# Kernel optimization log

Measured on AMD Instinct MI355X. Metric: run time of the kernel, lower is better.

## Reference

```python
import jax, jax.numpy as jnp
import numpy as np

NUM_GRAPHS = 512


def setup_inputs() -> dict:
    key = jax.random.key(0)
    k1, k2, k3, k4, k5, k6, k7 = jax.random.split(key, 7)
    N, E, D_IN, D_H = 100000, 3200000, 384, 64
    x_sem = jax.random.normal(k1, (N, D_IN), dtype=jnp.float32)
    edge_index = jax.random.randint(k2, (2, E), 0, N, dtype=jnp.int64)
    batch_index = jnp.sort(jax.random.randint(k3, (N,), 0, NUM_GRAPHS, dtype=jnp.int64))
    # GCNConv params: linear (no bias) + separate bias; classifier Linear(D_H, 1)
    W_gcn = jax.random.normal(k4, (D_IN, D_H), dtype=jnp.float32) / np.sqrt(D_IN)
    b_gcn = jnp.zeros((D_H,), dtype=jnp.float32)
    W_cls = jax.random.normal(k5, (D_H, 1), dtype=jnp.float32) / np.sqrt(D_H)
    b_cls = jnp.zeros((1,), dtype=jnp.float32)
    return {"x_sem": x_sem, "edge_index": edge_index, "batch_index": batch_index,
            "W_gcn": W_gcn, "b_gcn": b_gcn, "W_cls": W_cls, "b_cls": b_cls}


def reference(x_sem, edge_index, batch_index, W_gcn, b_gcn, W_cls, b_cls):
    N = x_sem.shape[0]
    # GCNConv: add self-loops, symmetric deg^{-1/2} A deg^{-1/2} normalization
    loop = jnp.arange(N, dtype=edge_index.dtype)
    src = jnp.concatenate([edge_index[0], loop])  # message source (x_j)
    dst = jnp.concatenate([edge_index[1], loop])  # aggregation target
    deg = jax.ops.segment_sum(jnp.ones_like(dst, dtype=x_sem.dtype), dst, num_segments=N)
    deg_inv_sqrt = jnp.where(deg > 0, jax.lax.rsqrt(jnp.maximum(deg, 1.0)), 0.0)
    norm = deg_inv_sqrt[src] * deg_inv_sqrt[dst]  # [E+N]
    h = x_sem @ W_gcn                                       # [N, D_H] project first (cheaper)
    msg = h[src] * norm[:, None]                            # gather + scale
    agg = jax.ops.segment_sum(msg, dst, num_segments=N) + b_gcn
    h = jax.nn.relu(agg)
    # global_add_pool over sorted batch_index
    z_graph = jax.ops.segment_sum(h, batch_index, num_segments=NUM_GRAPHS)  # [G, D_H]
    logits = z_graph @ W_cls + b_cls                        # [G, 1]
    return jnp.squeeze(logits, axis=-1)                     # [G]
```

## Files before the change

### kernel.cpp

```cpp
#include <hip/hip_runtime.h>
#include <hip/hip_bf16.h>

#define D_IN 384
#define D_H  64
#define BSH  7
#define BN   128
#define NBLK 512
#define EBUF 4608

typedef __attribute__((ext_vector_type(8))) short short8;
typedef __attribute__((ext_vector_type(4))) float f32x4;

__device__ __forceinline__ unsigned f2bf(float f){
  unsigned u = __float_as_uint(f);
  u += 0x7fffu + ((u >> 16) & 1u);
  return u >> 16;
}
__device__ __forceinline__ float bf2f(unsigned short u){
  return __uint_as_float((unsigned)u << 16);
}

__global__ __launch_bounds__(256) void k_bcount2(const int* __restrict__ ei,
                                                 int* __restrict__ hists,
                                                 int E, int NB, int chunk){
  __shared__ int hist[1024];
  const int blk = blockIdx.x;
  const int t = threadIdx.x;
  for (int i = t; i < NB; i += 256) hist[i] = 0;
  __syncthreads();
  const int cs = blk * chunk;
  const int ce = min(E, cs + chunk);
  for (int e = cs + t; e < ce; e += 256)
    atomicAdd(&hist[ei[E + e] >> BSH], 1);
  __syncthreads();
  for (int i = t; i < NB; i += 256)
    hists[(size_t)blk * NB + i] = hist[i];
}

__global__ __launch_bounds__(NBLK) void k_blkscan(const int* __restrict__ hists,
                                                  int* __restrict__ offs,
                                                  int* __restrict__ bsum, int NB){
  __shared__ int sd[NBLK];
  const int b = blockIdx.x;
  const int t = threadIdx.x;
  int c = hists[(size_t)t * NB + b];
  sd[t] = c;
  __syncthreads();
  for (int off = 1; off < NBLK; off <<= 1){
    int v = (t >= off) ? sd[t - off] : 0;
    __syncthreads();
    sd[t] += v;
    __syncthreads();
  }
  offs[(size_t)b * NBLK + t] = sd[t] - c;
  if (t == NBLK - 1) bsum[b] = sd[t];
}

__global__ __launch_bounds__(1024) void k_bscan(const int* __restrict__ bsum,
                                                int* bstart, int NB, int E){
  __shared__ int sd[1024];
  int t = threadIdx.x;
  int c = (t < NB) ? bsum[t] : 0;
  sd[t] = c;
  __syncthreads();
  for (int off = 1; off < 1024; off <<= 1){
    int v = (t >= off) ? sd[t - off] : 0;
    __syncthreads();
    sd[t] += v;
    __syncthreads();
  }
  if (t < NB) bstart[t] = sd[t] - c;
  if (t == 0) bstart[NB] = E;
}

__global__ __launch_bounds__(256) void k_bscatter2(const int* __restrict__ ei,
                                                   const int* __restrict__ bstart,
                                                   const int* __restrict__ offs,
                                                   unsigned* __restrict__ bscat,
                                                   int E, int NB, int chunk){
  __shared__ int lcur[1024];
  const int blk = blockIdx.x;
  const int t = threadIdx.x;
  for (int i = t; i < NB; i += 256)
    lcur[i] = bstart[i] + offs[(size_t)i * NBLK + blk];
  __syncthreads();
  const int cs = blk * chunk;
  const int ce = min(E, cs + chunk);
  for (int e = cs + t; e < ce; e += 256){
    int s = ei[e];
    int d = ei[E + e];
    int b = d >> BSH;
    int pos = atomicAdd(&lcur[b], 1);
    bscat[pos] = ((unsigned)(d & (BN - 1)) << 17) | (unsigned)s;
  }
}

__global__ __launch_bounds__(256) void k_nodecsr(const unsigned* __restrict__ bscat,
                                                 const int* __restrict__ bstart,
                                                 int* __restrict__ csr,
                                                 int* __restrict__ rowstart,
                                                 float* __restrict__ dis,
                                                 int N, int NB, int E){
  __shared__ int lcnt[BN];
  __shared__ int sc[BN];
  __shared__ int lcur[BN];
  __shared__ unsigned ebuf[EBUF];
  const int b = blockIdx.x;
  const int t = threadIdx.x;
  const int es = bstart[b], ee = bstart[b + 1];
  const int cnt = ee - es;

  if (t < BN) lcnt[t] = 0;
  __syncthreads();
  for (int i = t; i < cnt; i += 256){
    unsigned p = bscat[es + i];
    if (i < EBUF) ebuf[i] = p;
    atomicAdd(&lcnt[p >> 17], 1);
  }
  __syncthreads();
  if (t < BN) sc[t] = lcnt[t];
  __syncthreads();
  for (int off = 1; off < BN; off <<= 1){
    int v = (t < BN && t >= off) ? sc[t - off] : 0;
    __syncthreads();
    if (t < BN) sc[t] += v;
    __syncthreads();
  }
  if (t < BN){
    int excl = sc[t] - lcnt[t];
    lcur[t] = excl;
    int node = b * BN + t;
    if (node < N){
      rowstart[node] = es + excl;
      dis[node] = rsqrtf((float)(lcnt[t] + 1));
    }
  }
  if (b == NB - 1 && t == 0) rowstart[N] = E;
  __syncthreads();
  for (int i = t; i < cnt; i += 256){
    unsigned p = (i < EBUF) ? ebuf[i] : bscat[es + i];
    int pos = atomicAdd(&lcur[p >> 17], 1);
    csr[es + pos] = (int)((p & 0x1FFFFu) << 7);
  }
}

__global__ void k_wconv(const float* __restrict__ W, uint4* __restrict__ bpre){
  int j = blockIdx.x * blockDim.x + threadIdx.x;
  if (j >= 3072) return;
  int id = j & 1023, c = j >> 10;
  int cl = id & 63, s = (id >> 6) & 3, tl = id >> 8;
  int k = c * 128 + s * 32 + ((cl >> 4) << 3);
  int n = tl * 16 + (cl & 15);
  const float* wp = &W[(size_t)k * D_H + n];
  uint4 qv;
  qv.x = f2bf(wp[0])   | (f2bf(wp[64])  << 16);
  qv.y = f2bf(wp[128]) | (f2bf(wp[192]) << 16);
  qv.z = f2bf(wp[256]) | (f2bf(wp[320]) << 16);
  qv.w = f2bf(wp[384]) | (f2bf(wp[448]) << 16);
  bpre[j] = qv;
}

__global__ __launch_bounds__(256) void k_gemm(const float* __restrict__ x,
                                              const uint4* __restrict__ bpre,
                                              const float* __restrict__ dis,
                                              unsigned short* __restrict__ hb, int N){
  const int t = threadIdx.x;
  const int w = t >> 6;
  const int l = t & 63;
  const int node0 = blockIdx.x * 64;
  const int row = node0 + w * 16 + (l & 15);
  const int rowc = row < N ? row : N - 1;
  const float* xr = x + (size_t)rowc * D_IN + ((l >> 4) << 3);

  f32x4 acc[4];
  #pragma unroll
  for (int nt = 0; nt < 4; nt++) acc[nt] = (f32x4){0.f, 0.f, 0.f, 0.f};

  #pragma unroll
  for (int c = 0; c < 3; c++){
    #pragma unroll
    for (int s = 0; s < 4; s++){
      const float* xp = xr + c * 128 + s * 32;
      float4 u0 = *(const float4*)xp;
      float4 u1 = *(const float4*)(xp + 4);
      uint4 pv;
      pv.x = f2bf(u0.x) | (f2bf(u0.y) << 16);
      pv.y = f2bf(u0.z) | (f2bf(u0.w) << 16);
      pv.z = f2bf(u1.x) | (f2bf(u1.y) << 16);
      pv.w = f2bf(u1.z) | (f2bf(u1.w) << 16);
      short8 a = *reinterpret_cast<short8*>(&pv);
      #pragma unroll
      for (int nt = 0; nt < 4; nt++){
        short8 b = *reinterpret_cast<const short8*>(&bpre[c * 1024 + (nt * 4 + s) * 64 + l]);
        acc[nt] = __builtin_amdgcn_mfma_f32_16x16x32_bf16(a, b, acc[nt], 0, 0, 0);
      }
    }
  }
  const int qd = l >> 4;
  const int col0 = l & 15;
  #pragma unroll
  for (int r = 0; r < 4; r++){
    int node = node0 + w * 16 + qd * 4 + r;
    if (node < N){
      float scale = dis[node];
      #pragma unroll
      for (int nt = 0; nt < 4; nt++)
        hb[(size_t)node * D_H + nt * 16 + col0] = (unsigned short)f2bf(acc[nt][r] * scale);
    }
  }
}

__global__ __launch_bounds__(256) void k_agg(const unsigned short* __restrict__ hb,
                                             const int* __restrict__ csr,
                                             const int* __restrict__ rowstart,
                                             const float* __restrict__ dis,
                                             const float* __restrict__ bg,
                                             float* __restrict__ hout, int N){
  int gid = blockIdx.x * 256 + (int)threadIdx.x;
  int i = __builtin_amdgcn_readfirstlane(gid >> 6);
  if (i >= N) return;
  const int l = threadIdx.x & 63;
  const int c4 = (l & 31) << 2;
  const int hsel = l >> 5;
  const char* hbb = (const char*)hb;
  float ax = 0.f, ay = 0.f;

  {
    unsigned u = *(const unsigned*)(hbb + ((size_t)(unsigned)i << 7) + c4);
    if (!hsel){
      ax += __uint_as_float(u << 16);
      ay += __uint_as_float(u & 0xffff0000u);
    }
  }
  int e = rowstart[i];
  const int re = rowstart[i + 1];
  for (; e + 8 <= re; e += 8){
    int b0 = csr[e + 0], b1 = csr[e + 1];
    int b2 = csr[e + 2], b3 = csr[e + 3];
    int b4 = csr[e + 4], b5 = csr[e + 5];
    int b6 = csr[e + 6], b7 = csr[e + 7];
    unsigned u0 = *(const unsigned*)(hbb + (size_t)(unsigned)(hsel ? b1 : b0) + c4);
    unsigned u1 = *(const unsigned*)(hbb + (size_t)(unsigned)(hsel ? b3 : b2) + c4);
    unsigned u2 = *(const unsigned*)(hbb + (size_t)(unsigned)(hsel ? b5 : b4) + c4);
    unsigned u3 = *(const unsigned*)(hbb + (size_t)(unsigned)(hsel ? b7 : b6) + c4);
    ax += __uint_as_float(u0 << 16);          ay += __uint_as_float(u0 & 0xffff0000u);
    ax += __uint_as_float(u1 << 16);          ay += __uint_as_float(u1 & 0xffff0000u);
    ax += __uint_as_float(u2 << 16);          ay += __uint_as_float(u2 & 0xffff0000u);
    ax += __uint_as_float(u3 << 16);          ay += __uint_as_float(u3 & 0xffff0000u);
  }
  for (; e + 2 <= re; e += 2){
    int b0 = csr[e], b1 = csr[e + 1];
    unsigned u = *(const unsigned*)(hbb + (size_t)(unsigned)(hsel ? b1 : b0) + c4);
    ax += __uint_as_float(u << 16);
    ay += __uint_as_float(u & 0xffff0000u);
  }
  if (e < re){
    int b0 = csr[e];
    unsigned u = *(const unsigned*)(hbb + (size_t)(unsigned)b0 + c4);
    if (!hsel){
      ax += __uint_as_float(u << 16);
      ay += __uint_as_float(u & 0xffff0000u);
    }
  }
  ax += __shfl_xor(ax, 32);
  ay += __shfl_xor(ay, 32);
  if (!hsel){
    float di = dis[i];
    float2 bb = *(const float2*)(bg + (c4 >> 1));
    float vx = ax * di + bb.x; vx = vx > 0.f ? vx : 0.f;
    float vy = ay * di + bb.y; vy = vy > 0.f ? vy : 0.f;
    float2 o = make_float2(vx, vy);
    *(float2*)((char*)hout + (((size_t)(unsigned)i) << 8) + (c4 << 1)) = o;
  }
}

__global__ void k_pool(const float* __restrict__ hout, const int* __restrict__ batch,
                       const float* __restrict__ wc, const float* __restrict__ bc,
                       float* __restrict__ out, int N, int G){
  int g = blockIdx.x;
  int t = threadIdx.x;
  int lo = 0, hi = N;
  while (lo < hi){ int m = (lo + hi) >> 1; if (batch[m] < g) lo = m + 1; else hi = m; }
  int start = lo;
  lo = start; hi = N;
  while (lo < hi){ int m = (lo + hi) >> 1; if (batch[m] < g + 1) lo = m + 1; else hi = m; }
  int end = lo;

  int f = t & 63;
  int r = t >> 6;
  float sum = 0.f;
  for (int i = start + r; i < end; i += 4) sum += hout[(size_t)i * D_H + f];
  __shared__ float red[256];
  red[t] = sum;
  __syncthreads();
  if (t < 64){
    float z = red[t] + red[t + 64] + red[t + 128] + red[t + 192];
    float p = z * wc[t];
    #pragma unroll
    for (int off = 32; off > 0; off >>= 1) p += __shfl_down(p, off);
    if (t == 0) out[g] = p + bc[0];
  }
}

extern "C" void kernel_launch(void* const* d_in, const int* in_sizes, int n_in,
                              void* d_out, int out_size, void* d_ws, size_t ws_size,
                              hipStream_t stream){
  const float* x     = (const float*)d_in[0];
  const int*   ei    = (const int*)d_in[1];
  const int*   batch = (const int*)d_in[2];
  const float* Wg    = (const float*)d_in[3];
  const float* bg    = (const float*)d_in[4];
  const float* wc    = (const float*)d_in[5];
  const float* bc    = (const float*)d_in[6];
  float* out = (float*)d_out;

  const int N = in_sizes[2];
  const int E = in_sizes[1] / 2;
  const int G = out_size;
  const int NB = (N + BN - 1) / BN;
  const int chunk = (E + NBLK - 1) / NBLK;

  char* ws = (char*)d_ws;
  size_t off = 0;
  auto alloc = [&](size_t bytes) -> void* {
    void* p = ws + off;
    off += (bytes + 255) & ~(size_t)255;
    return p;
  };
  int*            hists    = (int*)           alloc((size_t)NBLK * NB * 4);
  int*            offs     = (int*)           alloc((size_t)NB * NBLK * 4);
  int*            bsum     = (int*)           alloc((size_t)NB * 4);
  int*            bstart   = (int*)           alloc((size_t)(NB + 1) * 4);
  unsigned*       bscat    = (unsigned*)      alloc((size_t)E * 4);
  int*            csr      = (int*)           alloc((size_t)E * 4);
  int*            rowstart = (int*)           alloc((size_t)(N + 1) * 4);
  float*          dis      = (float*)         alloc((size_t)N * 4);
  uint4*          bpre     = (uint4*)         alloc((size_t)3072 * 16);
  unsigned short* hb       = (unsigned short*)alloc((size_t)N * D_H * 2);
  float*          hout     = (float*)         alloc((size_t)N * D_H * 4);

  k_wconv    <<<12, 256, 0, stream>>>(Wg, bpre);
  k_bcount2  <<<NBLK, 256, 0, stream>>>(ei, hists, E, NB, chunk);
  k_blkscan  <<<NB, NBLK, 0, stream>>>(hists, offs, bsum, NB);
  k_bscan    <<<1, 1024, 0, stream>>>(bsum, bstart, NB, E);
  k_bscatter2<<<NBLK, 256, 0, stream>>>(ei, bstart, offs, bscat, E, NB, chunk);
  k_nodecsr  <<<NB, 256, 0, stream>>>(bscat, bstart, csr, rowstart, dis, N, NB, E);
  k_gemm     <<<(N + 63) / 64, 256, 0, stream>>>(x, bpre, dis, hb, N);
  k_agg      <<<(N + 3) / 4, 256, 0, stream>>>(hb, csr, rowstart, dis, bg, hout, N);
  k_pool     <<<G, 256, 0, stream>>>(hout, batch, wc, bc, out, N, G);
}
```

Measured before the change: 439.9 us.

## Fuse pooling and classifier into aggregation with atomics; widen gather lanes

Removes the separate pooling kernel and the fp32 hidden buffer. Each node's ReLU output is dotted with the classifier weights inside the aggregation kernel and added into its graph's output with one atomic, after a small kernel seeds the output with the bias. The gather is also reorganised so each wavefront handles four edges at a time, with 16 lanes per edge each loading 8 bytes, unrolled to 16 edges per iteration. The costs are 100k atomics onto 512 addresses, which can contend, and a summation order that is no longer deterministic.

```diff
diff --git a/kernel.cpp b/kernel.cpp
--- a/kernel.cpp
+++ b/kernel.cpp
@@ -16,8 +16,10 @@
   u += 0x7fffu + ((u >> 16) & 1u);
   return u >> 16;
 }
-__device__ __forceinline__ float bf2f(unsigned short u){
-  return __uint_as_float((unsigned)u << 16);
+
+__global__ void k_oinit(float* out, const float* __restrict__ bc, int G){
+  int g = blockIdx.x * blockDim.x + threadIdx.x;
+  if (g < G) out[g] = bc[0];
 }
 
 __global__ __launch_bounds__(256) void k_bcount2(const int* __restrict__ ei,
@@ -215,90 +217,80 @@
                                              const int* __restrict__ rowstart,
                                              const float* __restrict__ dis,
                                              const float* __restrict__ bg,
-                                             float* __restrict__ hout, int N){
+                                             const int* __restrict__ batch,
+                                             const float* __restrict__ wc,
+                                             float* __restrict__ out, int N){
   int gid = blockIdx.x * 256 + (int)threadIdx.x;
   int i = __builtin_amdgcn_readfirstlane(gid >> 6);
   if (i >= N) return;
   const int l = threadIdx.x & 63;
-  const int c4 = (l & 31) << 2;
-  const int hsel = l >> 5;
+  const int g = l >> 4;
+  const int fo = (l & 15) << 3;
   const char* hbb = (const char*)hb;
-  float ax = 0.f, ay = 0.f;
+  float a0 = 0.f, a1 = 0.f, a2 = 0.f, a3 = 0.f;
 
   {
-    unsigned u = *(const unsigned*)(hbb + ((size_t)(unsigned)i << 7) + c4);
-    if (!hsel){
-      ax += __uint_as_float(u << 16);
-      ay += __uint_as_float(u & 0xffff0000u);
-    }
-  }
-  int e = rowstart[i];
+    uint2 u = *(const uint2*)(hbb + ((size_t)(unsigned)i << 7) + fo);
+    if (g == 0){
+      a0 += __uint_as_float(u.x << 16);
+      a1 += __uint_as_float(u.x & 0xffff0000u);
+      a2 += __uint_as_float(u.y << 16);
+      a3 += __uint_as_float(u.y & 0xffff0000u);
+    }
+  }
+  const int rs = rowstart[i];
   const int re = rowstart[i + 1];
-  for (; e + 8 <= re; e += 8){
-    int b0 = csr[e + 0], b1 = csr[e + 1];
-    int b2 = csr[e + 2], b3 = csr[e + 3];
-    int b4 = csr[e + 4], b5 = csr[e + 5];
-    int b6 = csr[e + 6], b7 = csr[e + 7];
-    unsigned u0 = *(const unsigned*)(hbb + (size_t)(unsigned)(hsel ? b1 : b0) + c4);
-    unsigned u1 = *(const unsigned*)(hbb + (size_t)(unsigned)(hsel ? b3 : b2) + c4);
-    unsigned u2 = *(const unsigned*)(hbb + (size_t)(unsigned)(hsel ? b5 : b4) + c4);
-    unsigned u3 = *(const unsigned*)(hbb + (size_t)(unsigned)(hsel ? b7 : b6) + c4);
-    ax += __uint_as_float(u0 << 16);          ay += __uint_as_float(u0 & 0xffff0000u);
-    ax += __uint_as_float(u1 << 16);          ay += __uint_as_float(u1 & 0xffff0000u);
-    ax += __uint_as_float(u2 << 16);          ay += __uint_as_float(u2 & 0xffff0000u);
-    ax += __uint_as_float(u3 << 16);          ay += __uint_as_float(u3 & 0xffff0000u);
-  }
-  for (; e + 2 <= re; e += 2){
-    int b0 = csr[e], b1 = csr[e + 1];
-    unsigned u = *(const unsigned*)(hbb + (size_t)(unsigned)(hsel ? b1 : b0) + c4);
-    ax += __uint_as_float(u << 16);
-    ay += __uint_as_float(u & 0xffff0000u);
-  }
-  if (e < re){
-    int b0 = csr[e];
-    unsigned u = *(const unsigned*)(hbb + (size_t)(unsigned)b0 + c4);
-    if (!hsel){
-      ax += __uint_as_float(u << 16);
-      ay += __uint_as_float(u & 0xffff0000u);
-    }
-  }
-  ax += __shfl_xor(ax, 32);
-  ay += __shfl_xor(ay, 32);
-  if (!hsel){
+  int e = rs;
+  for (; e + 16 <= re; e += 16){
+    int b0 = csr[e + g];
+    int b1 = csr[e + 4 + g];
+    int b2 = csr[e + 8 + g];
+    int b3 = csr[e + 12 + g];
+    uint2 u0 = *(const uint2*)(hbb + (size_t)(unsigned)b0 + fo);
+    uint2 u1 = *(const uint2*)(hbb + (size_t)(unsigned)b1 + fo);
+    uint2 u2 = *(const uint2*)(hbb + (size_t)(unsigned)b2 + fo);
+    uint2 u3 = *(const uint2*)(hbb + (size_t)(unsigned)b3 + fo);
+    a0 += __uint_as_float(u0.x << 16);  a1 += __uint_as_float(u0.x & 0xffff0000u);
+    a2 += __uint_as_float(u0.y << 16);  a3 += __uint_as_float(u0.y & 0xffff0000u);
+    a0 += __uint_as_float(u1.x << 16);  a1 += __uint_as_float(u1.x & 0xffff0000u);
+    a2 += __uint_as_float(u1.y << 16);  a3 += __uint_as_float(u1.y & 0xffff0000u);
+    a0 += __uint_as_float(u2.x << 16);  a1 += __uint_as_float(u2.x & 0xffff0000u);
+    a2 += __uint_as_float(u2.y << 16);  a3 += __uint_as_float(u2.y & 0xffff0000u);
+    a0 += __uint_as_float(u3.x << 16);  a1 += __uint_as_float(u3.x & 0xffff0000u);
+    a2 += __uint_as_float(u3.y << 16);  a3 += __uint_as_float(u3.y & 0xffff0000u);
+  }
+  for (; e < re; e += 4){
+    int idx = e + g;
+    bool val = idx < re;
+    int b = csr[val ? idx : rs];
+    uint2 u = *(const uint2*)(hbb + (size_t)(unsigned)b + fo);
+    if (val){
+      a0 += __uint_as_float(u.x << 16);
+      a1 += __uint_as_float(u.x & 0xffff0000u);
+      a2 += __uint_as_float(u.y << 16);
+      a3 += __uint_as_float(u.y & 0xffff0000u);
+    }
+  }
+  a0 += __shfl_xor(a0, 16); a0 += __shfl_xor(a0, 32);
+  a1 += __shfl_xor(a1, 16); a1 += __shfl_xor(a1, 32);
+  a2 += __shfl_xor(a2, 16); a2 += __shfl_xor(a2, 32);
+  a3 += __shfl_xor(a3, 16); a3 += __shfl_xor(a3, 32);
+
+  if (g == 0){
     float di = dis[i];
-    float2 bb = *(const float2*)(bg + (c4 >> 1));
-    float vx = ax * di + bb.x; vx = vx > 0.f ? vx : 0.f;
-    float vy = ay * di + bb.y; vy = vy > 0.f ? vy : 0.f;
-    float2 o = make_float2(vx, vy);
-    *(float2*)((char*)hout + (((size_t)(unsigned)i) << 8) + (c4 << 1)) = o;
-  }
-}
-
-__global__ void k_pool(const float* __restrict__ hout, const int* __restrict__ batch,
-                       const float* __restrict__ wc, const float* __restrict__ bc,
-                       float* __restrict__ out, int N, int G){
-  int g = blockIdx.x;
-  int t = threadIdx.x;
-  int lo = 0, hi = N;
-  while (lo < hi){ int m = (lo + hi) >> 1; if (batch[m] < g) lo = m + 1; else hi = m; }
-  int start = lo;
-  lo = start; hi = N;
-  while (lo < hi){ int m = (lo + hi) >> 1; if (batch[m] < g + 1) lo = m + 1; else hi = m; }
-  int end = lo;
-
-  int f = t & 63;
-  int r = t >> 6;
-  float sum = 0.f;
-  for (int i = start + r; i < end; i += 4) sum += hout[(size_t)i * D_H + f];
-  __shared__ float red[256];
-  red[t] = sum;
-  __syncthreads();
-  if (t < 64){
-    float z = red[t] + red[t + 64] + red[t + 128] + red[t + 192];
-    float p = z * wc[t];
-    #pragma unroll
-    for (int off = 32; off > 0; off >>= 1) p += __shfl_down(p, off);
-    if (t == 0) out[g] = p + bc[0];
+    int f0 = (l & 15) << 2;
+    float4 bb = *(const float4*)(bg + f0);
+    float4 ww = *(const float4*)(wc + f0);
+    float v0 = a0 * di + bb.x; v0 = v0 > 0.f ? v0 : 0.f;
+    float v1 = a1 * di + bb.y; v1 = v1 > 0.f ? v1 : 0.f;
+    float v2 = a2 * di + bb.z; v2 = v2 > 0.f ? v2 : 0.f;
+    float v3 = a3 * di + bb.w; v3 = v3 > 0.f ? v3 : 0.f;
+    float s = v0 * ww.x + v1 * ww.y + v2 * ww.z + v3 * ww.w;
+    s += __shfl_xor(s, 1);
+    s += __shfl_xor(s, 2);
+    s += __shfl_xor(s, 4);
+    s += __shfl_xor(s, 8);
+    if (l == 0) atomicAdd(&out[batch[i]], s);
   }
 }
 
@@ -337,8 +329,8 @@
   float*          dis      = (float*)         alloc((size_t)N * 4);
   uint4*          bpre     = (uint4*)         alloc((size_t)3072 * 16);
   unsigned short* hb       = (unsigned short*)alloc((size_t)N * D_H * 2);
-  float*          hout     = (float*)         alloc((size_t)N * D_H * 4);
-
+
+  k_oinit    <<<(G + 255) / 256, 256, 0, stream>>>(out, bc, G);
   k_wconv    <<<12, 256, 0, stream>>>(Wg, bpre);
   k_bcount2  <<<NBLK, 256, 0, stream>>>(ei, hists, E, NB, chunk);
   k_blkscan  <<<NB, NBLK, 0, stream>>>(hists, offs, bsum, NB);
@@ -346,6 +338,5 @@
   k_bscatter2<<<NBLK, 256, 0, stream>>>(ei, bstart, offs, bscat, E, NB, chunk);
   k_nodecsr  <<<NB, 256, 0, stream>>>(bscat, bstart, csr, rowstart, dis, N, NB, E);
   k_gemm     <<<(N + 63) / 64, 256, 0, stream>>>(x, bpre, dis, hb, N);
-  k_agg      <<<(N + 3) / 4, 256, 0, stream>>>(hb, csr, rowstart, dis, bg, hout, N);
-  k_pool     <<<G, 256, 0, stream>>>(hout, batch, wc, bc, out, N, G);
-}
+  k_agg      <<<(N + 3) / 4, 256, 0, stream>>>(hb, csr, rowstart, dis, bg, batch, wc, out, N);
+}
```

Result: slower. 587.2 us (+33.5%).

## Fuse global pooling and classifier into aggregation kernel via atomics

Applied to the files above, without the earlier changes.

The aggregation kernel now applies the classifier weights to each node's ReLU output, reduces across the 32 lanes with shuffles, and atomically adds the scalar into the per-graph output. A small init kernel first seeds the output with the classifier bias. This drops the N x 64 float hout buffer write and the separate pooling kernel with its binary searches and re-read. The cost is one float atomic per node into 512 slots, which adds contention and makes the summation order nondeterministic.

```diff
diff --git a/kernel.cpp b/kernel.cpp
--- a/kernel.cpp
+++ b/kernel.cpp
@@ -16,8 +16,10 @@
   u += 0x7fffu + ((u >> 16) & 1u);
   return u >> 16;
 }
-__device__ __forceinline__ float bf2f(unsigned short u){
-  return __uint_as_float((unsigned)u << 16);
+
+__global__ void k_oinit(float* out, const float* __restrict__ bc, int G){
+  int g = blockIdx.x * blockDim.x + threadIdx.x;
+  if (g < G) out[g] = bc[0];
 }
 
 __global__ __launch_bounds__(256) void k_bcount2(const int* __restrict__ ei,
@@ -215,7 +217,9 @@
                                              const int* __restrict__ rowstart,
                                              const float* __restrict__ dis,
                                              const float* __restrict__ bg,
-                                             float* __restrict__ hout, int N){
+                                             const int* __restrict__ batch,
+                                             const float* __restrict__ wc,
+                                             float* __restrict__ out, int N){
   int gid = blockIdx.x * 256 + (int)threadIdx.x;
   int i = __builtin_amdgcn_readfirstlane(gid >> 6);
   if (i >= N) return;
@@ -266,39 +270,18 @@
   ay += __shfl_xor(ay, 32);
   if (!hsel){
     float di = dis[i];
-    float2 bb = *(const float2*)(bg + (c4 >> 1));
+    int f0 = (l & 31) << 1;
+    float2 bb = *(const float2*)(bg + f0);
+    float2 ww = *(const float2*)(wc + f0);
     float vx = ax * di + bb.x; vx = vx > 0.f ? vx : 0.f;
     float vy = ay * di + bb.y; vy = vy > 0.f ? vy : 0.f;
-    float2 o = make_float2(vx, vy);
-    *(float2*)((char*)hout + (((size_t)(unsigned)i) << 8) + (c4 << 1)) = o;
-  }
-}
-
-__global__ void k_pool(const float* __restrict__ hout, const int* __restrict__ batch,
-                       const float* __restrict__ wc, const float* __restrict__ bc,
-                       float* __restrict__ out, int N, int G){
-  int g = blockIdx.x;
-  int t = threadIdx.x;
-  int lo = 0, hi = N;
-  while (lo < hi){ int m = (lo + hi) >> 1; if (batch[m] < g) lo = m + 1; else hi = m; }
-  int start = lo;
-  lo = start; hi = N;
-  while (lo < hi){ int m = (lo + hi) >> 1; if (batch[m] < g + 1) lo = m + 1; else hi = m; }
-  int end = lo;
-
-  int f = t & 63;
-  int r = t >> 6;
-  float sum = 0.f;
-  for (int i = start + r; i < end; i += 4) sum += hout[(size_t)i * D_H + f];
-  __shared__ float red[256];
-  red[t] = sum;
-  __syncthreads();
-  if (t < 64){
-    float z = red[t] + red[t + 64] + red[t + 128] + red[t + 192];
-    float p = z * wc[t];
-    #pragma unroll
-    for (int off = 32; off > 0; off >>= 1) p += __shfl_down(p, off);
-    if (t == 0) out[g] = p + bc[0];
+    float s = vx * ww.x + vy * ww.y;
+    s += __shfl_xor(s, 1);
+    s += __shfl_xor(s, 2);
+    s += __shfl_xor(s, 4);
+    s += __shfl_xor(s, 8);
+    s += __shfl_xor(s, 16);
+    if (l == 0) atomicAdd(&out[batch[i]], s);
   }
 }
 
@@ -337,8 +320,8 @@
   float*          dis      = (float*)         alloc((size_t)N * 4);
   uint4*          bpre     = (uint4*)         alloc((size_t)3072 * 16);
   unsigned short* hb       = (unsigned short*)alloc((size_t)N * D_H * 2);
-  float*          hout     = (float*)         alloc((size_t)N * D_H * 4);
-
+
+  k_oinit    <<<(G + 255) / 256, 256, 0, stream>>>(out, bc, G);
   k_wconv    <<<12, 256, 0, stream>>>(Wg, bpre);
   k_bcount2  <<<NBLK, 256, 0, stream>>>(ei, hists, E, NB, chunk);
   k_blkscan  <<<NB, NBLK, 0, stream>>>(hists, offs, bsum, NB);
@@ -346,6 +329,5 @@
   k_bscatter2<<<NBLK, 256, 0, stream>>>(ei, bstart, offs, bscat, E, NB, chunk);
   k_nodecsr  <<<NB, 256, 0, stream>>>(bscat, bstart, csr, rowstart, dis, N, NB, E);
   k_gemm     <<<(N + 63) / 64, 256, 0, stream>>>(x, bpre, dis, hb, N);
-  k_agg      <<<(N + 3) / 4, 256, 0, stream>>>(hb, csr, rowstart, dis, bg, hout, N);
-  k_pool     <<<G, 256, 0, stream>>>(hout, batch, wc, bc, out, N, G);
-}
+  k_agg      <<<(N + 3) / 4, 256, 0, stream>>>(hb, csr, rowstart, dis, bg, batch, wc, out, N);
+}
```

Measured after the change: 620.7 us. +41.1%, slower.
